# Optimization experiments

Measured on AMD Instinct MI355X. Metric: run time of the kernel, lower is better.

Reference implementation:

```python
import jax, jax.numpy as jnp
import numpy as np

D_MODEL = 1024
NUM_HEADS = 16
D_K = D_MODEL // NUM_HEADS
B, T = 2, 2048


def setup_inputs() -> dict:
    key = jax.random.key(0)
    ks = jax.random.split(key, 11)
    s = 1.0 / np.sqrt(D_MODEL)
    inp = {
        "q": jax.random.normal(ks[0], (B, T, D_MODEL), jnp.float32),
        "k": jax.random.normal(ks[1], (B, T, D_MODEL), jnp.float32),
        "v": jax.random.normal(ks[2], (B, T, D_MODEL), jnp.float32),
        "mask": jnp.tril(jnp.ones((1, 1, T, T), jnp.int32)),  # causal
        "wq": jax.random.normal(ks[3], (D_MODEL, D_MODEL), jnp.float32) * s,
        "bq": jnp.zeros((D_MODEL,), jnp.float32),
        "wk": jax.random.normal(ks[4], (D_MODEL, D_MODEL), jnp.float32) * s,
        "bk": jnp.zeros((D_MODEL,), jnp.float32),
        "wv": jax.random.normal(ks[5], (D_MODEL, D_MODEL), jnp.float32) * s,
        "bv": jnp.zeros((D_MODEL,), jnp.float32),
        "wo": jax.random.normal(ks[6], (D_MODEL, D_MODEL), jnp.float32) * s,
        "bo": jnp.zeros((D_MODEL,), jnp.float32),
    }
    return inp


def reference(q, k, v, mask, wq, bq, wk, bk, wv, bv, wo, bo):
    Bq, Tq, _ = q.shape
    Tk = k.shape[1]
    # projections, split into heads: (B, H, T, d_k)
    qh = (q @ wq + bq).reshape(Bq, Tq, NUM_HEADS, D_K).transpose(0, 2, 1, 3)
    kh = (k @ wk + bk).reshape(Bq, Tk, NUM_HEADS, D_K).transpose(0, 2, 1, 3)
    vh = (v @ wv + bv).reshape(Bq, Tk, NUM_HEADS, D_K).transpose(0, 2, 1, 3)
    scores = jnp.einsum("bhqd,bhkd->bhqk", qh, kh) / jnp.sqrt(jnp.float32(D_K))
    scores = jnp.where(mask == 0, jnp.float32(-1e9), scores)
    attn = jax.nn.softmax(scores, axis=-1)
    ctx = jnp.einsum("bhqk,bhkd->bhqd", attn, vh)
    ctx = ctx.transpose(0, 2, 1, 3).reshape(Bq, Tq, D_MODEL)
    return ctx @ wo + bo
```

## Files before the change

kernel.cpp:

```cpp
#include <hip/hip_runtime.h>
#include <hip/hip_bf16.h>

#define DM 1024
#define NH 16
#define DK 64
#define TT 2048
#define BATCH 2

typedef __attribute__((ext_vector_type(8))) short bf16x8;
typedef __attribute__((ext_vector_type(4))) float f32x4;
typedef __attribute__((ext_vector_type(4))) unsigned short u16x4;
typedef unsigned short u16;

__device__ inline u16 f2b(float x){ __hip_bfloat16 h = __float2bfloat16(x); return *reinterpret_cast<u16*>(&h); }

__device__ inline void gl_lds16(const u16* g, u16* l) {
  __builtin_amdgcn_global_load_lds(
      (const __attribute__((address_space(1))) unsigned int*)g,
      (__attribute__((address_space(3))) unsigned int*)l, 16, 0, 0);
}

__global__ __launch_bounds__(256) void prep(const float* __restrict__ q, const float* __restrict__ k,
                                            const float* __restrict__ v,
                                            const float* __restrict__ wq, const float* __restrict__ wk,
                                            const float* __restrict__ wv, const float* __restrict__ wo,
                                            u16* __restrict__ qb, u16* __restrict__ kb,
                                            u16* __restrict__ vb, u16* __restrict__ wt) {
  int z = blockIdx.z;
  if (z < 3) {
    const float* src = z==0 ? q : z==1 ? k : v;
    u16* dst = z==0 ? qb : z==1 ? kb : vb;
    size_t i = ((size_t)blockIdx.x*256 + threadIdx.x)*8;
    f32x4 a = *(const f32x4*)(src+i);
    f32x4 b = *(const f32x4*)(src+i+4);
    union { bf16x8 v8; u16 e[8]; } u;
    #pragma unroll
    for (int j=0;j<4;j++){ u.e[j] = f2b(a[j]); u.e[4+j] = f2b(b[j]); }
    *(bf16x8*)(dst+i) = u.v8;
  } else {
    int bx = blockIdx.x;
    if (bx >= 1024) return;
    __shared__ float tile[32][33];
    const float* src = z==3 ? wq : z==4 ? wk : z==5 ? wv : wo;
    u16* dst = wt + (size_t)(z-3)*DM*DM;
    int bxx = bx & 31, byy = bx >> 5;
    int tx = threadIdx.x & 31, ty = threadIdx.x >> 5;
    int x  = bxx*32 + tx;
    int y0 = byy*32 + ty;
    #pragma unroll
    for (int i=0;i<32;i+=8) tile[ty+i][tx] = src[(size_t)(y0+i)*DM + x];
    __syncthreads();
    int xo = byy*32 + tx;
    int yo = bxx*32 + ty;
    #pragma unroll
    for (int i=0;i<32;i+=8) dst[(size_t)(yo+i)*DM + xo] = f2b(tile[tx][ty+i]);
  }
}

__global__ __launch_bounds__(512, 2) void gemm_qkv(const u16* __restrict__ qb, const u16* __restrict__ kb,
                                                   const u16* __restrict__ vb, const u16* __restrict__ wt,
                                                   const float* __restrict__ bq, const float* __restrict__ bk,
                                                   const float* __restrict__ bv,
                                                   u16* __restrict__ qh, u16* __restrict__ kh,
                                                   u16* __restrict__ vhT) {
  const int bid = blockIdx.x;
  const int swz = (bid & 7)*24 + (bid >> 3);
  const int z  = swz >> 6;
  const int rb = swz & 63;
  const int row0 = (rb >> 2) * 256;
  const int col0 = (rb & 3) * 256;

  const u16* A = z==0 ? qb : z==1 ? kb : vb;
  const u16* W = wt + (size_t)z*DM*DM;
  const float* bias = z==0 ? bq : z==1 ? bk : bv;
  u16* outv = z==0 ? qh : z==1 ? kh : vhT;
  const int mode = (z==2);
  const float oscale = (z==0) ? 0.125f : 1.0f;

  __shared__ __align__(16) u16 As[2][16384];
  __shared__ __align__(16) u16 Bs[2][16384];

  const int tid = threadIdx.x, lane = tid & 63, wid = tid >> 6;
  const int li = lane & 15, quad = lane >> 4, l7 = lane & 7;
  const int wr = wid >> 2, wc = wid & 3;

  int r_[2], gs_[2];
  #pragma unroll
  for (int c=0;c<2;c++){ int idx = tid + c*512; int rr = idx>>3; int gd = idx&7; r_[c]=rr; gs_[c]=gd^(rr&7); }

  auto stage = [&](int op, int t, int hf, int slot){
    const u16* base = op ? W : A;
    const int rowbase = (op ? col0 : row0) + hf*128;
    u16* lb = (op ? Bs[slot] : As[slot]) + hf*8192;
    #pragma unroll
    for (int c=0;c<2;c++){
      gl_lds16(base + (size_t)(rowbase + r_[c])*DM + t*64 + gs_[c]*8,
               lb + ((wid*64 + c*512) << 3));
    }
  };

  f32x4 acc[8][4];
  #pragma unroll
  for (int i=0;i<8;i++)
    #pragma unroll
    for (int j=0;j<4;j++) acc[i][j] = f32x4{0.f,0.f,0.f,0.f};

  stage(1, 0, 0, 0); stage(1, 0, 1, 0);
  stage(0, 0, 0, 0); stage(0, 0, 1, 0);
  stage(1, 1, 0, 1); stage(1, 1, 1, 1);
  asm volatile("s_waitcnt vmcnt(4)" ::: "memory");
  __builtin_amdgcn_s_barrier();

  bf16x8 b[4][2];
  for (int i = 0; i < 8; i++) {
    const int t2 = 2*i;
    #pragma unroll
    for (int half = 0; half < 2; half++) {
      const int slot = half;
      #pragma unroll
      for (int q = 0; q < 4; q++) {
        if (q == 0) {
          const u16* bb = Bs[slot] + (wc>>1)*8192 + (wc&1)*4096;
          #pragma unroll
          for (int c=0;c<4;c++)
            #pragma unroll
            for (int kh=0;kh<2;kh++)
              b[c][kh] = *(const bf16x8*)&bb[(c*16 + li)*64 + ((quad + 4*kh) ^ l7)*8];
        }
        bf16x8 a[2][2];
        {
          const u16* ab = As[slot] + wr*8192;
          #pragma unroll
          for (int rr2=0; rr2<2; rr2++)
            #pragma unroll
            for (int kh=0;kh<2;kh++)
              a[rr2][kh] = *(const bf16x8*)&ab[((q*2+rr2)*16 + li)*64 + ((quad + 4*kh) ^ l7)*8];
        }
        {
          const int sop = (q >= 2);
          const int st  = t2 + 1 + half + (q >= 2);
          const int shf = q & 1;
          const int ssl = (q >= 2) ? half : (1 - half);
          if (st <= 15) stage(sop, st, shf, ssl);
        }
        if (q == 0) asm volatile("s_waitcnt lgkmcnt(8)" ::: "memory");
        __builtin_amdgcn_s_barrier();
        asm volatile("s_waitcnt lgkmcnt(0)" ::: "memory");
        __builtin_amdgcn_sched_barrier(0);
        __builtin_amdgcn_s_setprio(1);
        #pragma unroll
        for (int rr2=0; rr2<2; rr2++)
          #pragma unroll
          for (int c=0;c<4;c++)
            #pragma unroll
            for (int kh=0;kh<2;kh++)
              acc[q*2+rr2][c] = __builtin_amdgcn_mfma_f32_16x16x32_bf16(a[rr2][kh], b[c][kh], acc[q*2+rr2][c], 0,0,0);
        __builtin_amdgcn_s_setprio(0);
        if (q == 3) {
          if (half == 0) {
            if (i < 7) asm volatile("s_waitcnt vmcnt(4)" ::: "memory");
            else       asm volatile("s_waitcnt vmcnt(0)" ::: "memory");
          } else {
            if (i < 7) asm volatile("s_waitcnt vmcnt(4)" ::: "memory");
          }
        }
        __builtin_amdgcn_s_barrier();
      }
    }
  }

  if (!mode) {
    #pragma unroll
    for (int c=0;c<4;c++) {
      int col = col0 + wc*64 + c*16 + li;
      float bsv = bias[col];
      #pragma unroll
      for (int fr=0; fr<8; fr++) {
        int rowb = row0 + wr*128 + fr*16 + quad*4;
        #pragma unroll
        for (int r=0;r<4;r++)
          outv[(size_t)(rowb + r)*DM + col] = f2b((acc[fr][c][r] + bsv) * oscale);
      }
    }
  } else {
    #pragma unroll
    for (int c=0;c<4;c++) {
      int col = col0 + wc*64 + c*16 + li;
      float bsv = bias[col];
      int hh = col >> 6, d = col & 63;
      #pragma unroll
      for (int fr=0; fr<8; fr++) {
        int rowb = row0 + wr*128 + fr*16 + quad*4;
        int bb = rowb >> 11, t0 = rowb & (TT-1);
        u16x4 w;
        #pragma unroll
        for (int r=0;r<4;r++) w[r] = f2b(acc[fr][c][r] + bsv);
        *(u16x4*)&outv[(((size_t)(bb*NH + hh)*DK + d)*TT) + t0] = w;
      }
    }
  }
}

__global__ __launch_bounds__(256) void gemm_out64(const u16* __restrict__ A, const u16* __restrict__ W,
                                                  const float* __restrict__ bias, float* __restrict__ out) {
  __shared__ __align__(16) u16 As[3][128*32];
  __shared__ __align__(16) u16 Bs[3][64*32];
  const int tid = threadIdx.x, lane = tid & 63, wid = tid >> 6;
  const int li = lane & 15, quad = lane >> 4;
  const int row0 = blockIdx.x*128, col0 = blockIdx.y*64;
  const int wr = wid & 1, wc = wid >> 1;

  const int srow = lane >> 2;
  const int scol = ((lane & 3) ^ ((srow >> 1) & 3)) * 8;
  const int rsw  = (li >> 1) & 3;

  auto stage = [&](int hh, int bufi) {
    const int kk = hh*32;
    #pragma unroll
    for (int c=0;c<2;c++) {
      int ch = wid*2 + c;
      gl_lds16(A + (size_t)(row0 + ch*16 + srow)*DM + kk + scol, &As[bufi][ch*512]);
    }
    gl_lds16(W + (size_t)(col0 + wid*16 + srow)*DM + kk + scol, &Bs[bufi][wid*512]);
  };

  f32x4 acc[4][2];
  #pragma unroll
  for (int i=0;i<4;i++)
    #pragma unroll
    for (int j=0;j<2;j++) acc[i][j] = f32x4{0.f,0.f,0.f,0.f};

  stage(0, 0);
  stage(1, 1);
  asm volatile("s_waitcnt vmcnt(3)" ::: "memory");
  __builtin_amdgcn_s_barrier();

  int buf = 0;
  for (int h = 0; h < 32; h++) {
    bf16x8 a[4], b[2];
    #pragma unroll
    for (int i=0;i<4;i++) a[i] = *(const bf16x8*)&As[buf][(wr*64 + i*16 + li)*32 + (quad ^ rsw)*8];
    #pragma unroll
    for (int j=0;j<2;j++) b[j] = *(const bf16x8*)&Bs[buf][(wc*32 + j*16 + li)*32 + (quad ^ rsw)*8];

    if (h < 30) { int nb = buf + 2; if (nb >= 3) nb -= 3; stage(h+2, nb); }

    __builtin_amdgcn_s_setprio(1);
    #pragma unroll
    for (int i=0;i<4;i++)
      #pragma unroll
      for (int j=0;j<2;j++)
        acc[i][j] = __builtin_amdgcn_mfma_f32_16x16x32_bf16(a[i], b[j], acc[i][j], 0,0,0);
    __builtin_amdgcn_s_setprio(0);

    if (h < 30)       asm volatile("s_waitcnt vmcnt(3)" ::: "memory");
    else if (h == 30) asm volatile("s_waitcnt vmcnt(0)" ::: "memory");
    __builtin_amdgcn_s_barrier();
    if (++buf == 3) buf = 0;
  }

  #pragma unroll
  for (int j=0;j<2;j++) {
    int col = col0 + wc*32 + j*16 + li;
    float bsv = bias[col];
    #pragma unroll
    for (int i=0;i<4;i++) {
      #pragma unroll
      for (int r=0;r<4;r++) {
        int row = row0 + wr*64 + i*16 + quad*4 + r;
        out[(size_t)row*DM + col] = acc[i][j][r] + bsv;
      }
    }
  }
}

__global__ __launch_bounds__(256) void flash(const u16* __restrict__ qh, const u16* __restrict__ kh,
                                             const u16* __restrict__ vhT, u16* __restrict__ ctx) {
  const int bh = blockIdx.x;
  const int pr = blockIdx.y;
  const int b = bh >> 4, h = bh & 15;
  const u16* Q  = qh  + (size_t)b*TT*DM + h*DK;
  const u16* K  = kh  + (size_t)b*TT*DM + h*DK;
  const u16* Vt = vhT + (size_t)bh*DK*TT;

  const int tid = threadIdx.x, lane = tid & 63, wid = tid >> 6;
  const int li = lane & 15, quad = lane >> 4;

  __shared__ u16 Kl[64][72];
  __shared__ u16 Vl[64][72];
  __shared__ u16 Pb[4][16][72];

  const int sr = tid >> 3;
  const int sc = (tid & 7) * 8;

  bf16x8 kr0 = *(const bf16x8*)&K[(size_t)(sr   )*DM + sc];
  bf16x8 kr1 = *(const bf16x8*)&K[(size_t)(sr+32)*DM + sc];
  bf16x8 vr0 = *(const bf16x8*)&Vt[(size_t)(sr   )*TT + sc];
  bf16x8 vr1 = *(const bf16x8*)&Vt[(size_t)(sr+32)*TT + sc];

  #pragma unroll
  for (int ph = 0; ph < 2; ph++) {
    const int qt = (ph == 0) ? pr : (31 - pr);
    const int nt = qt + 1;
    const int qrow0 = qt*64 + wid*16;

    bf16x8 qf0 = *(const bf16x8*)&Q[(size_t)(qrow0+li)*DM +      quad*8];
    bf16x8 qf1 = *(const bf16x8*)&Q[(size_t)(qrow0+li)*DM + 32 + quad*8];

    f32x4 o[4];
    #pragma unroll
    for (int d=0;d<4;d++) o[d] = f32x4{0.f,0.f,0.f,0.f};
    float lp = 0.f;

    for (int it = 0; it < nt; it++) {
      const int k0 = it*64;
      __syncthreads();
      *(bf16x8*)&Kl[sr   ][sc] = kr0;
      *(bf16x8*)&Kl[sr+32][sc] = kr1;
      *(bf16x8*)&Vl[sr   ][sc] = vr0;
      *(bf16x8*)&Vl[sr+32][sc] = vr1;
      __syncthreads();
      if (it+1 < nt) {
        const int k1 = k0 + 64;
        kr0 = *(const bf16x8*)&K[(size_t)(k1+sr   )*DM + sc];
        kr1 = *(const bf16x8*)&K[(size_t)(k1+sr+32)*DM + sc];
        vr0 = *(const bf16x8*)&Vt[(size_t)(sr   )*TT + k1 + sc];
        vr1 = *(const bf16x8*)&Vt[(size_t)(sr+32)*TT + k1 + sc];
      } else if (ph == 0) {
        kr0 = *(const bf16x8*)&K[(size_t)(sr   )*DM + sc];
        kr1 = *(const bf16x8*)&K[(size_t)(sr+32)*DM + sc];
        vr0 = *(const bf16x8*)&Vt[(size_t)(sr   )*TT + sc];
        vr1 = *(const bf16x8*)&Vt[(size_t)(sr+32)*TT + sc];
      }

      f32x4 s[4];
      #pragma unroll
      for (int c=0;c<4;c++) {
        bf16x8 kf0 = *(const bf16x8*)&Kl[c*16+li][     quad*8];
        bf16x8 kf1 = *(const bf16x8*)&Kl[c*16+li][32 + quad*8];
        f32x4 t = __builtin_amdgcn_mfma_f32_16x16x32_bf16(kf0, qf0, f32x4{0.f,0.f,0.f,0.f}, 0,0,0);
        s[c]    = __builtin_amdgcn_mfma_f32_16x16x32_bf16(kf1, qf1, t, 0,0,0);
      }
      const bool dg = (it == nt-1);
      const int qq = qrow0 + li;
      float p[4][4];
      if (dg) {
        #pragma unroll
        for (int c=0;c<4;c++)
          #pragma unroll
          for (int r=0;r<4;r++){
            int key = k0 + c*16 + quad*4 + r;
            p[c][r] = (key <= qq) ? __expf(s[c][r]) : 0.f;
          }
      } else {
        #pragma unroll
        for (int c=0;c<4;c++)
          #pragma unroll
          for (int r=0;r<4;r++)
            p[c][r] = __expf(s[c][r]);
      }
      #pragma unroll
      for (int c=0;c<4;c++)
        #pragma unroll
        for (int r=0;r<4;r++)
          lp += p[c][r];

      #pragma unroll
      for (int c=0;c<4;c++) {
        u16x4 w;
        #pragma unroll
        for (int r=0;r<4;r++) w[r] = f2b(p[c][r]);
        *(u16x4*)&Pb[wid][li][c*16 + quad*4] = w;
      }
      __builtin_amdgcn_wave_barrier();
      __asm__ __volatile__("s_waitcnt lgkmcnt(0)");
      bf16x8 pf0 = *(const bf16x8*)&Pb[wid][li][     quad*8];
      bf16x8 pf1 = *(const bf16x8*)&Pb[wid][li][32 + quad*8];

      #pragma unroll
      for (int d=0;d<4;d++){
        bf16x8 vf0 = *(const bf16x8*)&Vl[d*16+li][     quad*8];
        bf16x8 vf1 = *(const bf16x8*)&Vl[d*16+li][32 + quad*8];
        o[d] = __builtin_amdgcn_mfma_f32_16x16x32_bf16(vf0, pf0, o[d], 0,0,0);
        o[d] = __builtin_amdgcn_mfma_f32_16x16x32_bf16(vf1, pf1, o[d], 0,0,0);
      }
    }

    lp += __shfl_xor(lp, 16, 64);
    lp += __shfl_xor(lp, 32, 64);
    float rl = 1.0f / lp;

    const int qq = qrow0 + li;
    #pragma unroll
    for (int d=0;d<4;d++){
      u16x4 w;
      #pragma unroll
      for (int r=0;r<4;r++) w[r] = f2b(o[d][r] * rl);
      *(u16x4*)&ctx[(size_t)(b*TT + qq)*DM + h*DK + d*16 + quad*4] = w;
    }
  }
}

extern "C" void kernel_launch(void* const* d_in, const int* in_sizes, int n_in,
                              void* d_out, int out_size, void* d_ws, size_t ws_size,
                              hipStream_t stream) {
  const float* q   = (const float*)d_in[0];
  const float* k   = (const float*)d_in[1];
  const float* v   = (const float*)d_in[2];
  const float* wq  = (const float*)d_in[4];
  const float* bq  = (const float*)d_in[5];
  const float* wk  = (const float*)d_in[6];
  const float* bk  = (const float*)d_in[7];
  const float* wv  = (const float*)d_in[8];
  const float* bv  = (const float*)d_in[9];
  const float* wo  = (const float*)d_in[10];
  const float* bo  = (const float*)d_in[11];
  float* out = (float*)d_out;

  const size_t SZ = (size_t)BATCH*TT*DM;
  u16* wt  = (u16*)d_ws;
  u16* qb  = wt + (size_t)4*DM*DM;
  u16* kb  = qb + SZ;
  u16* vb  = kb + SZ;
  u16* qh  = vb + SZ;
  u16* kh  = qh + SZ;
  u16* vhT = kh + SZ;
  u16* ctx = qb;

  prep<<<dim3(2048, 1, 7), 256, 0, stream>>>(q, k, v, wq, wk, wv, wo, qb, kb, vb, wt);

  gemm_qkv<<<dim3(192, 1, 1), 512, 0, stream>>>(qb, kb, vb, wt, bq, bk, bv, qh, kh, vhT);

  flash<<<dim3(BATCH*NH, 16), 256, 0, stream>>>(qh, kh, vhT, ctx);

  gemm_out64<<<dim3(4096/128, DM/64), 256, 0, stream>>>(ctx, wt + (size_t)3*DM*DM, bo, out);
}
```

Measured before the change: 222.3 us.

## Use 128-row query tiles with two subtiles per wave and XOR-swizzled LDS

```diff
diff --git a/kernel.cpp b/kernel.cpp
--- a/kernel.cpp
+++ b/kernel.cpp
@@ -277,125 +277,147 @@
 __global__ __launch_bounds__(256) void flash(const u16* __restrict__ qh, const u16* __restrict__ kh,
                                              const u16* __restrict__ vhT, u16* __restrict__ ctx) {
   const int bh = blockIdx.x;
-  const int pr = blockIdx.y;
+  const int qt = 15 - blockIdx.y;
   const int b = bh >> 4, h = bh & 15;
   const u16* Q  = qh  + (size_t)b*TT*DM + h*DK;
   const u16* K  = kh  + (size_t)b*TT*DM + h*DK;
   const u16* Vt = vhT + (size_t)bh*DK*TT;
 
   const int tid = threadIdx.x, lane = tid & 63, wid = tid >> 6;
-  const int li = lane & 15, quad = lane >> 4;
-
-  __shared__ u16 Kl[64][72];
-  __shared__ u16 Vl[64][72];
-  __shared__ u16 Pb[4][16][72];
+  const int li = lane & 15, quad = lane >> 4, l7 = lane & 7;
+
+  __shared__ __align__(16) u16 Kl[64][64];
+  __shared__ __align__(16) u16 Vl[64][64];
+  __shared__ __align__(16) u16 Pb[4][16][64];
 
   const int sr = tid >> 3;
-  const int sc = (tid & 7) * 8;
-
-  bf16x8 kr0 = *(const bf16x8*)&K[(size_t)(sr   )*DM + sc];
-  bf16x8 kr1 = *(const bf16x8*)&K[(size_t)(sr+32)*DM + sc];
-  bf16x8 vr0 = *(const bf16x8*)&Vt[(size_t)(sr   )*TT + sc];
-  bf16x8 vr1 = *(const bf16x8*)&Vt[(size_t)(sr+32)*TT + sc];
-
-  #pragma unroll
-  for (int ph = 0; ph < 2; ph++) {
-    const int qt = (ph == 0) ? pr : (31 - pr);
-    const int nt = qt + 1;
-    const int qrow0 = qt*64 + wid*16;
-
-    bf16x8 qf0 = *(const bf16x8*)&Q[(size_t)(qrow0+li)*DM +      quad*8];
-    bf16x8 qf1 = *(const bf16x8*)&Q[(size_t)(qrow0+li)*DM + 32 + quad*8];
-
-    f32x4 o[4];
-    #pragma unroll
-    for (int d=0;d<4;d++) o[d] = f32x4{0.f,0.f,0.f,0.f};
-    float lp = 0.f;
-
-    for (int it = 0; it < nt; it++) {
-      const int k0 = it*64;
-      __syncthreads();
-      *(bf16x8*)&Kl[sr   ][sc] = kr0;
-      *(bf16x8*)&Kl[sr+32][sc] = kr1;
-      *(bf16x8*)&Vl[sr   ][sc] = vr0;
-      *(bf16x8*)&Vl[sr+32][sc] = vr1;
-      __syncthreads();
-      if (it+1 < nt) {
-        const int k1 = k0 + 64;
-        kr0 = *(const bf16x8*)&K[(size_t)(k1+sr   )*DM + sc];
-        kr1 = *(const bf16x8*)&K[(size_t)(k1+sr+32)*DM + sc];
-        vr0 = *(const bf16x8*)&Vt[(size_t)(sr   )*TT + k1 + sc];
-        vr1 = *(const bf16x8*)&Vt[(size_t)(sr+32)*TT + k1 + sc];
-      } else if (ph == 0) {
-        kr0 = *(const bf16x8*)&K[(size_t)(sr   )*DM + sc];
-        kr1 = *(const bf16x8*)&K[(size_t)(sr+32)*DM + sc];
-        vr0 = *(const bf16x8*)&Vt[(size_t)(sr   )*TT + sc];
-        vr1 = *(const bf16x8*)&Vt[(size_t)(sr+32)*TT + sc];
-      }
-
-      f32x4 s[4];
+  const int sg = tid & 7;
+  const int ssl = (sg ^ (sr & 7)) * 8;
+
+  const int nt  = 2*qt + 2;
+  const int qw0 = qt*128 + wid*32;
+
+  bf16x8 qf[2][2];
+  #pragma unroll
+  for (int su=0; su<2; su++)
+    #pragma unroll
+    for (int k2=0; k2<2; k2++)
+      qf[su][k2] = *(const bf16x8*)&Q[(size_t)(qw0 + su*16 + li)*DM + k2*32 + quad*8];
+
+  f32x4 o[2][4];
+  #pragma unroll
+  for (int su=0; su<2; su++)
+    #pragma unroll
+    for (int d=0; d<4; d++) o[su][d] = f32x4{0.f,0.f,0.f,0.f};
+  float lp[2] = {0.f, 0.f};
+
+  bf16x8 kr0 = *(const bf16x8*)&K[(size_t)(sr   )*DM + sg*8];
+  bf16x8 kr1 = *(const bf16x8*)&K[(size_t)(sr+32)*DM + sg*8];
+  bf16x8 vr0 = *(const bf16x8*)&Vt[(size_t)(sr   )*TT + sg*8];
+  bf16x8 vr1 = *(const bf16x8*)&Vt[(size_t)(sr+32)*TT + sg*8];
+
+  for (int it = 0; it < nt; it++) {
+    const int k0 = it*64;
+    __syncthreads();
+    *(bf16x8*)&Kl[sr   ][ssl] = kr0;
+    *(bf16x8*)&Kl[sr+32][ssl] = kr1;
+    *(bf16x8*)&Vl[sr   ][ssl] = vr0;
+    *(bf16x8*)&Vl[sr+32][ssl] = vr1;
+    __syncthreads();
+    if (it+1 < nt) {
+      const int k1 = k0 + 64;
+      kr0 = *(const bf16x8*)&K[(size_t)(k1+sr   )*DM + sg*8];
+      kr1 = *(const bf16x8*)&K[(size_t)(k1+sr+32)*DM + sg*8];
+      vr0 = *(const bf16x8*)&Vt[(size_t)(sr   )*TT + k1 + sg*8];
+      vr1 = *(const bf16x8*)&Vt[(size_t)(sr+32)*TT + k1 + sg*8];
+    }
+
+    if (k0 <= qw0 + 31) {
+      f32x4 s[2][4];
+      __builtin_amdgcn_s_setprio(1);
       #pragma unroll
       for (int c=0;c<4;c++) {
-        bf16x8 kf0 = *(const bf16x8*)&Kl[c*16+li][     quad*8];
-        bf16x8 kf1 = *(const bf16x8*)&Kl[c*16+li][32 + quad*8];
-        f32x4 t = __builtin_amdgcn_mfma_f32_16x16x32_bf16(kf0, qf0, f32x4{0.f,0.f,0.f,0.f}, 0,0,0);
-        s[c]    = __builtin_amdgcn_mfma_f32_16x16x32_bf16(kf1, qf1, t, 0,0,0);
-      }
-      const bool dg = (it == nt-1);
-      const int qq = qrow0 + li;
-      float p[4][4];
-      if (dg) {
+        bf16x8 kf0 = *(const bf16x8*)&Kl[c*16+li][((quad    ) ^ l7)*8];
+        bf16x8 kf1 = *(const bf16x8*)&Kl[c*16+li][((quad + 4) ^ l7)*8];
         #pragma unroll
-        for (int c=0;c<4;c++)
-          #pragma unroll
-          for (int r=0;r<4;r++){
-            int key = k0 + c*16 + quad*4 + r;
-            p[c][r] = (key <= qq) ? __expf(s[c][r]) : 0.f;
+        for (int su=0; su<2; su++) {
+          f32x4 t = __builtin_amdgcn_mfma_f32_16x16x32_bf16(kf0, qf[su][0], f32x4{0.f,0.f,0.f,0.f}, 0,0,0);
+          s[su][c] = __builtin_amdgcn_mfma_f32_16x16x32_bf16(kf1, qf[su][1], t, 0,0,0);
+        }
+      }
+      __builtin_amdgcn_s_setprio(0);
+
+      bf16x8 vf[4][2];
+      #pragma unroll
+      for (int d=0; d<4; d++) {
+        vf[d][0] = *(const bf16x8*)&Vl[d*16+li][((quad    ) ^ l7)*8];
+        vf[d][1] = *(const bf16x8*)&Vl[d*16+li][((quad + 4) ^ l7)*8];
+      }
+
+      #pragma unroll
+      for (int su=0; su<2; su++) {
+        const int qr = qw0 + su*16;
+        if (k0 <= qr + 15) {
+          const int qq = qr + li;
+          float p[4][4];
+          if (k0 + 63 > qr) {
+            #pragma unroll
+            for (int c=0;c<4;c++)
+              #pragma unroll
+              for (int r=0;r<4;r++){
+                int key = k0 + c*16 + quad*4 + r;
+                p[c][r] = (key <= qq) ? __expf(s[su][c][r]) : 0.f;
+              }
+          } else {
+            #pragma unroll
+            for (int c=0;c<4;c++)
+              #pragma unroll
+              for (int r=0;r<4;r++)
+                p[c][r] = __expf(s[su][c][r]);
           }
-      } else {
-        #pragma unroll
-        for (int c=0;c<4;c++)
-          #pragma unroll
-          for (int r=0;r<4;r++)
-            p[c][r] = __expf(s[c][r]);
-      }
-      #pragma unroll
-      for (int c=0;c<4;c++)
-        #pragma unroll
-        for (int r=0;r<4;r++)
-          lp += p[c][r];
-
-      #pragma unroll
-      for (int c=0;c<4;c++) {
-        u16x4 w;
-        #pragma unroll
-        for (int r=0;r<4;r++) w[r] = f2b(p[c][r]);
-        *(u16x4*)&Pb[wid][li][c*16 + quad*4] = w;
-      }
-      __builtin_amdgcn_wave_barrier();
-      __asm__ __volatile__("s_waitcnt lgkmcnt(0)");
-      bf16x8 pf0 = *(const bf16x8*)&Pb[wid][li][     quad*8];
-      bf16x8 pf1 = *(const bf16x8*)&Pb[wid][li][32 + quad*8];
-
-      #pragma unroll
-      for (int d=0;d<4;d++){
-        bf16x8 vf0 = *(const bf16x8*)&Vl[d*16+li][     quad*8];
-        bf16x8 vf1 = *(const bf16x8*)&Vl[d*16+li][32 + quad*8];
-        o[d] = __builtin_amdgcn_mfma_f32_16x16x32_bf16(vf0, pf0, o[d], 0,0,0);
-        o[d] = __builtin_amdgcn_mfma_f32_16x16x32_bf16(vf1, pf1, o[d], 0,0,0);
-      }
-    }
-
-    lp += __shfl_xor(lp, 16, 64);
-    lp += __shfl_xor(lp, 32, 64);
-    float rl = 1.0f / lp;
-
-    const int qq = qrow0 + li;
+          #pragma unroll
+          for (int c=0;c<4;c++)
+            #pragma unroll
+            for (int r=0;r<4;r++)
+              lp[su] += p[c][r];
+
+          #pragma unroll
+          for (int c=0;c<4;c++) {
+            u16x4 w;
+            #pragma unroll
+            for (int r=0;r<4;r++) w[r] = f2b(p[c][r]);
+            const int gc = c*2 + (quad>>1);
+            *(u16x4*)&Pb[wid][li][((gc ^ l7)*8) + (quad&1)*4] = w;
+          }
+          __builtin_amdgcn_wave_barrier();
+          __asm__ __volatile__("s_waitcnt lgkmcnt(0)");
+          bf16x8 pf0 = *(const bf16x8*)&Pb[wid][li][((quad    ) ^ l7)*8];
+          bf16x8 pf1 = *(const bf16x8*)&Pb[wid][li][((quad + 4) ^ l7)*8];
+
+          __builtin_amdgcn_s_setprio(1);
+          #pragma unroll
+          for (int d=0;d<4;d++){
+            o[su][d] = __builtin_amdgcn_mfma_f32_16x16x32_bf16(vf[d][0], pf0, o[su][d], 0,0,0);
+            o[su][d] = __builtin_amdgcn_mfma_f32_16x16x32_bf16(vf[d][1], pf1, o[su][d], 0,0,0);
+          }
+          __builtin_amdgcn_s_setprio(0);
+        }
+      }
+    }
+  }
+
+  #pragma unroll
+  for (int su=0; su<2; su++) {
+    float lpv = lp[su];
+    lpv += __shfl_xor(lpv, 16, 64);
+    lpv += __shfl_xor(lpv, 32, 64);
+    float rl = 1.0f / lpv;
+    const int qq = qw0 + su*16 + li;
     #pragma unroll
     for (int d=0;d<4;d++){
       u16x4 w;
       #pragma unroll
-      for (int r=0;r<4;r++) w[r] = f2b(o[d][r] * rl);
+      for (int r=0;r<4;r++) w[r] = f2b(o[su][d][r] * rl);
       *(u16x4*)&ctx[(size_t)(b*TT + qq)*DM + h*DK + d*16 + quad*4] = w;
     }
   }
```

Result: no change. 224.6 us (+1.0%).
